# Kernel tuning notes

Hardware: AMD Instinct MI355X
Metric: run time of the kernel (lower is better)

The kernel has to match this reference:

```python
import jax, jax.numpy as jnp
import numpy as np

B, T, DIN, DC, CS = 8, 4096, 1024, 256, 8192
EPS = 1e-12

def _l2norm(x):
    # F.normalize: x / max(||x||_2, eps) along last axis
    n = jnp.sqrt(jnp.sum(x * x, axis=-1, keepdims=True))
    return x / jnp.maximum(n, EPS)

def _wn(v, g):
    # torch weight_norm(dim=0): w = g * v / ||v|| per output row
    n = jnp.sqrt(jnp.sum(v * v, axis=1, keepdims=True))
    return g * v / jnp.maximum(n, EPS)

def setup_inputs() -> dict:
    key = jax.random.key(0)
    k = jax.random.split(key, 4)
    return {
        "z": jax.random.normal(k[0], (B, DIN, T), jnp.float32),
        "in_v": jax.random.normal(k[1], (DC, DIN), jnp.float32) * 0.02,
        "in_g": jnp.ones((DC, 1), jnp.float32),
        "in_b": jnp.zeros((DC,), jnp.float32),
        "out_v": jax.random.normal(k[2], (DIN, DC), jnp.float32) * 0.02,
        "out_g": jnp.ones((DIN, 1), jnp.float32),
        "out_b": jnp.zeros((DIN,), jnp.float32),
        "codebook": jax.random.normal(k[3], (CS, DC), jnp.float32),
    }

def reference(z, in_v, in_g, in_b, out_v, out_g, out_b, codebook):
    b, _, t = z.shape
    w_in = _wn(in_v, in_g)                      # (DC, DIN)
    z_e = jnp.einsum('bdt,cd->bct', z, w_in) + in_b[None, :, None]  # (B, DC, T)

    # decode_latents (eval mode: dropout p=0)
    enc = _l2norm(z_e.transpose(0, 2, 1).reshape(b * t, -1))   # (BT, DC)
    cb = _l2norm(codebook)                                     # (CS, DC)
    dist = (jnp.sum(enc * enc, axis=1, keepdims=True)
            - 2.0 * enc @ cb.T
            + jnp.sum(cb * cb, axis=1)[None, :])               # (BT, CS)
    indices = jnp.argmax(-dist, axis=1).reshape(b, t)          # (B, T)
    z_q = codebook[indices].transpose(0, 2, 1)                 # (B, DC, T)

    commitment_loss = jnp.mean((z_e - jax.lax.stop_gradient(z_q)) ** 2, axis=(1, 2))
    codebook_loss = jnp.mean((z_q - jax.lax.stop_gradient(z_e)) ** 2, axis=(1, 2))

    z_q_st = z_e + jax.lax.stop_gradient(z_q - z_e)            # straight-through
    w_out = _wn(out_v, out_g)                                  # (DIN, DC)
    z_q_out = jnp.einsum('bct,dc->bdt', z_q_st, w_out) + out_b[None, :, None]
    return (z_q_out, commitment_loss, codebook_loss, indices)
```

## Files before the change

### kernel.cpp

```cpp
#include <hip/hip_runtime.h>
#include <stdint.h>

#define BB 8
#define TT 4096
#define DIN 1024
#define DC 256
#define CS 8192
#define EPSF 1e-12f

typedef unsigned short ushort_t;
typedef __attribute__((ext_vector_type(8))) short short8;
typedef __attribute__((ext_vector_type(4))) float f32x4;

constexpr size_t OFF_WIN   = 0;
constexpr size_t OFF_WOUTT = OFF_WIN   + 1048576;
constexpr size_t OFF_CBN   = OFF_WOUTT + 1048576;
constexpr size_t OFF_NRM2  = OFF_CBN   + 8388608;
constexpr size_t OFF_ZE    = OFF_NRM2  + 32768;
constexpr size_t OFF_INV   = OFF_ZE    + 33554432;
constexpr size_t OFF_ENC2  = OFF_INV   + 131072;
constexpr size_t OFF_KEYS  = OFF_ENC2  + 131072;
constexpr size_t OFF_LOSS  = OFF_KEYS  + 262144;
constexpr size_t OFF_WSPL  = OFF_LOSS  + 256;
constexpr size_t OFF_W2T   = OFF_WSPL  + 1048576;
constexpr size_t REQ_WS_ZE = OFF_W2T + 134217728ull;

__device__ __forceinline__ float block_reduce_sum_256(float v, float* sbuf) {
  #pragma unroll
  for (int o = 32; o > 0; o >>= 1) v += __shfl_down(v, o, 64);
  int lane = threadIdx.x & 63, w = threadIdx.x >> 6;
  if (lane == 0) sbuf[w] = v;
  __syncthreads();
  float r = sbuf[0] + sbuf[1] + sbuf[2] + sbuf[3];
  __syncthreads();
  return r;
}

__device__ __forceinline__ ushort_t bf16_rne(float x) {
  unsigned u = __float_as_uint(x);
  unsigned r = (u + 0x7FFFu + ((u >> 16) & 1u)) >> 16;
  return (ushort_t)r;
}
__device__ __forceinline__ float bf16f(ushort_t h) {
  return __uint_as_float(((unsigned)h) << 16);
}

__device__ __forceinline__ void async_copy16(const ushort_t* g, ushort_t* lds) {
  __builtin_amdgcn_global_load_lds(
      (const __attribute__((address_space(1))) void*)g,
      (__attribute__((address_space(3))) void*)lds, 16, 0, 0);
}

__device__ __forceinline__ void stage_tile(const ushort_t* __restrict__ s0, int ld,
                                           ushort_t* __restrict__ dstbuf, int rr, int cc) {
  #pragma unroll
  for (int r16 = 0; r16 < 8; r16++) {
    int r = r16*16 + rr;
    int g = cc ^ ((r + (r >> 2)) & 3);
    async_copy16(s0 + (size_t)r*ld + (g << 3), dstbuf + r16*512);
  }
}

__device__ __forceinline__ void stage_comp(const ushort_t* __restrict__ src,
                                           ushort_t* __restrict__ comp, int tid) {
  const int lane = tid & 63;
  const int wb = tid - lane;
  #pragma unroll
  for (int l = 0; l < 2; l++) {
    int chunk = l*512 + wb + lane;
    int r = chunk >> 2, c = chunk & 3;
    int g = c ^ ((r + (r >> 2)) & 3);
    async_copy16(src + (size_t)r*DC + (g << 3),
                 comp + (size_t)(l*512 + wb)*8);
  }
}

#define LD8(base, off) (*(const short8*)((const char*)(base) + (off)))

template<int MH, int CLO>
__device__ __forceinline__ void qmfma(f32x4 (&acc)[8][4],
    const short8 (&fah)[4], const short8 (&fal)[4],
    const short8 (&fbh)[4], const short8 (&fbl)[4]) {
  #pragma unroll
  for (int r = 0; r < 4; r++) {
    #pragma unroll
    for (int c2 = 0; c2 < 2; c2++) {
      f32x4 t = acc[MH*4 + r][CLO + c2];
      t = __builtin_amdgcn_mfma_f32_16x16x32_bf16(fah[r], fbh[CLO + c2], t, 0, 0, 0);
      t = __builtin_amdgcn_mfma_f32_16x16x32_bf16(fal[r], fbh[CLO + c2], t, 0, 0, 0);
      t = __builtin_amdgcn_mfma_f32_16x16x32_bf16(fah[r], fbl[CLO + c2], t, 0, 0, 0);
      acc[MH*4 + r][CLO + c2] = t;
    }
  }
}

__global__ void k_prep_win(const float* __restrict__ v, const float* __restrict__ g,
                           float* __restrict__ w, ushort_t* __restrict__ wh,
                           ushort_t* __restrict__ wl) {
  __shared__ float sb[4];
  int r = blockIdx.x, t = threadIdx.x;
  float xv[4]; float s = 0.f;
  #pragma unroll
  for (int i = 0; i < 4; i++) { xv[i] = v[r*DIN + t + i*256]; s += xv[i]*xv[i]; }
  s = block_reduce_sum_256(s, sb);
  float sc = g[r] / fmaxf(sqrtf(s), EPSF);
  #pragma unroll
  for (int i = 0; i < 4; i++) {
    float val = xv[i] * sc;
    int idx = r*DIN + t + i*256;
    w[idx] = val;
    ushort_t h = bf16_rne(val);
    wh[idx] = h;
    wl[idx] = bf16_rne(val - bf16f(h));
  }
}

__global__ void k_prep_wout(const float* __restrict__ v, const float* __restrict__ g,
                            float* __restrict__ wT) {
  __shared__ float sb[4];
  int r = blockIdx.x, t = threadIdx.x;
  float x = v[r*DC + t];
  float s = block_reduce_sum_256(x*x, sb);
  float sc = g[r] / fmaxf(sqrtf(s), EPSF);
  wT[t*DIN + r] = x * sc;
}

__global__ void k_prep_cb(const float* __restrict__ cb, ushort_t* __restrict__ cbh,
                          ushort_t* __restrict__ cbl, float* __restrict__ nrm2) {
  __shared__ float sb[4];
  int j = blockIdx.x, t = threadIdx.x;
  float x = cb[j*DC + t];
  float s = block_reduce_sum_256(x*x, sb);
  float nm = fmaxf(sqrtf(s), EPSF);
  float cn = x / nm;
  ushort_t h = bf16_rne(cn);
  cbh[j*DC + t] = h;
  cbl[j*DC + t] = bf16_rne(cn - bf16f(h));
  float q = block_reduce_sum_256(cn*cn, sb);
  if (t == 0) nrm2[j] = q;
}

template<bool BIAS>
__global__ __launch_bounds__(256) void k_gemm(
    const float* __restrict__ A, const float* __restrict__ Bmat,
    const float* __restrict__ bias, float* __restrict__ C,
    int K, int lda, int ldb, int ldc, size_t strideB, size_t strideC)
{
  __shared__ float As[16][132];
  __shared__ float Bs[16][132];
  const int bn = blockIdx.x * 128;
  const int bm = blockIdx.y * 128;
  const float* Bb = Bmat + (size_t)blockIdx.z * strideB;
  float* Cb = C + (size_t)blockIdx.z * strideC;
  const int tid = threadIdx.x;
  const int tx = tid & 15, ty = tid >> 4;
  const int am = tid & 127, akq = (tid >> 7) * 8;
  const int bk = tid >> 5, bj = (tid & 31) * 4;

  float acc[8][8];
  #pragma unroll
  for (int i = 0; i < 8; i++)
    #pragma unroll
    for (int j = 0; j < 8; j++) acc[i][j] = 0.f;

  for (int k0 = 0; k0 < K; k0 += 16) {
    float4 a0 = *(const float4*)&A[(size_t)(bm+am)*lda + k0 + akq];
    float4 a1 = *(const float4*)&A[(size_t)(bm+am)*lda + k0 + akq + 4];
    float4 b0 = *(const float4*)&Bb[(size_t)(k0+bk)*ldb + bn + bj];
    float4 b1 = *(const float4*)&Bb[(size_t)(k0+bk+8)*ldb + bn + bj];
    As[akq+0][am] = a0.x; As[akq+1][am] = a0.y; As[akq+2][am] = a0.z; As[akq+3][am] = a0.w;
    As[akq+4][am] = a1.x; As[akq+5][am] = a1.y; As[akq+6][am] = a1.z; As[akq+7][am] = a1.w;
    *(float4*)&Bs[bk][bj] = b0;
    *(float4*)&Bs[bk+8][bj] = b1;
    __syncthreads();
    #pragma unroll
    for (int k = 0; k < 16; k++) {
      float av[8], bv[8];
      float4 x0 = *(const float4*)&As[k][tx*4];
      float4 x1 = *(const float4*)&As[k][tx*4+64];
      float4 y0 = *(const float4*)&Bs[k][ty*4];
      float4 y1 = *(const float4*)&Bs[k][ty*4+64];
      av[0]=x0.x; av[1]=x0.y; av[2]=x0.z; av[3]=x0.w;
      av[4]=x1.x; av[5]=x1.y; av[6]=x1.z; av[7]=x1.w;
      bv[0]=y0.x; bv[1]=y0.y; bv[2]=y0.z; bv[3]=y0.w;
      bv[4]=y1.x; bv[5]=y1.y; bv[6]=y1.z; bv[7]=y1.w;
      #pragma unroll
      for (int i = 0; i < 8; i++)
        #pragma unroll
        for (int j = 0; j < 8; j++)
          acc[i][j] += av[i] * bv[j];
    }
    __syncthreads();
  }

  #pragma unroll
  for (int i = 0; i < 8; i++) {
    int mm = bm + ((i < 4) ? tx*4 + i : 64 + tx*4 + (i-4));
    float bia = BIAS ? bias[mm] : 0.f;
    float4 v0 = make_float4(acc[i][0]+bia, acc[i][1]+bia, acc[i][2]+bia, acc[i][3]+bia);
    float4 v1 = make_float4(acc[i][4]+bia, acc[i][5]+bia, acc[i][6]+bia, acc[i][7]+bia);
    *(float4*)&Cb[(size_t)mm*ldc + bn + ty*4]      = v0;
    *(float4*)&Cb[(size_t)mm*ldc + bn + 64 + ty*4] = v1;
  }
}

__global__ void k_split_z(const float* __restrict__ z, ushort_t* __restrict__ zhi,
                          ushort_t* __restrict__ zlo) {
  __shared__ float tile[64][65];
  int b = blockIdx.z, t0 = blockIdx.x * 64, d0 = blockIdx.y * 64;
  int tx = threadIdx.x & 63, ty = threadIdx.x >> 6;
  const float* zb = z + (size_t)b*DIN*TT;
  #pragma unroll
  for (int i = 0; i < 16; i++) {
    int d = i*4 + ty;
    tile[d][tx] = zb[(size_t)(d0+d)*TT + t0 + tx];
  }
  __syncthreads();
  #pragma unroll
  for (int i = 0; i < 16; i++) {
    int t = i*4 + ty;
    float val = tile[tx][t];
    ushort_t h = bf16_rne(val);
    size_t o = ((size_t)(b*TT + t0 + t))*DIN + d0 + tx;
    zhi[o] = h;
    zlo[o] = bf16_rne(val - bf16f(h));
  }
}

__global__ __launch_bounds__(256) void k_ze_mfma(
    const ushort_t* __restrict__ zth, const ushort_t* __restrict__ ztl,
    const ushort_t* __restrict__ wh, const ushort_t* __restrict__ wl,
    const float* __restrict__ in_b, float* __restrict__ ze)
{
  __shared__ ushort_t As_hi[2][4096];
  __shared__ ushort_t As_lo[2][4096];
  __shared__ ushort_t Bs_hi[2][4096];
  __shared__ ushort_t Bs_lo[2][4096];

  const int b  = blockIdx.z;
  const int t0 = blockIdx.x * 128;
  const int c0 = blockIdx.y * 128;
  const int tid = threadIdx.x;
  const int lane = tid & 63;
  const int wave = tid >> 6;
  const int wr = wave >> 1, wc = wave & 1;
  const int m = lane & 15, quad = lane >> 4;

  const ushort_t* src; ushort_t* dst;
  {
    size_t aoff = ((size_t)(b*TT + t0)) * DIN;
    size_t boff = (size_t)c0 * DIN;
    if      (wave == 0) { src = zth + aoff; dst = &As_hi[0][0]; }
    else if (wave == 1) { src = ztl + aoff; dst = &As_lo[0][0]; }
    else if (wave == 2) { src = wh + boff;  dst = &Bs_hi[0][0]; }
    else                { src = wl + boff;  dst = &Bs_lo[0][0]; }
  }
  const int rr = lane >> 2, cc = lane & 3;

  int offA[4], offB[4];
  #pragma unroll
  for (int ri = 0; ri < 4; ri++) {
    int r = wr*64 + ri*16 + m;
    int p = quad ^ ((r + (r >> 2)) & 3);
    offA[ri] = r*64 + p*16;
  }
  #pragma unroll
  for (int ci = 0; ci < 4; ci++) {
    int r = wc*64 + ci*16 + m;
    int p = quad ^ ((r + (r >> 2)) & 3);
    offB[ci] = r*64 + p*16;
  }

  f32x4 acc[4][4];
  #pragma unroll
  for (int i = 0; i < 4; i++)
    #pragma unroll
    for (int j = 0; j < 4; j++) acc[i][j] = (f32x4)0.f;

  stage_tile(src, DIN, dst, rr, cc);

  for (int it = 0; it < 32; ++it) {
    __syncthreads();
    if (it < 31) stage_tile(src + (it+1)*32, DIN, dst + ((it+1)&1)*4096, rr, cc);
    const int bo = (it & 1) << 13;

    short8 bh[4], bl[4];
    #pragma unroll
    for (int ci = 0; ci < 4; ci++) {
      bh[ci] = *(const short8*)((const char*)Bs_hi + bo + offB[ci]);
      bl[ci] = *(const short8*)((const char*)Bs_lo + bo + offB[ci]);
    }
    #pragma unroll
    for (int ri = 0; ri < 4; ri++) {
      short8 ah = *(const short8*)((const char*)As_hi + bo + offA[ri]);
      short8 al = *(const short8*)((const char*)As_lo + bo + offA[ri]);
      #pragma unroll
      for (int ci = 0; ci < 4; ci++) {
        acc[ri][ci] = __builtin_amdgcn_mfma_f32_16x16x32_bf16(ah, bh[ci], acc[ri][ci], 0, 0, 0);
        acc[ri][ci] = __builtin_amdgcn_mfma_f32_16x16x32_bf16(al, bh[ci], acc[ri][ci], 0, 0, 0);
        acc[ri][ci] = __builtin_amdgcn_mfma_f32_16x16x32_bf16(ah, bl[ci], acc[ri][ci], 0, 0, 0);
      }
    }
  }

  #pragma unroll
  for (int ri = 0; ri < 4; ri++) {
    int t_loc = wr*64 + ri*16 + quad*4;
    #pragma unroll
    for (int ci = 0; ci < 4; ci++) {
      int c_loc = wc*64 + ci*16 + m;
      float bia = in_b[c0 + c_loc];
      float4 v = make_float4(acc[ri][ci][0]+bia, acc[ri][ci][1]+bia,
                             acc[ri][ci][2]+bia, acc[ri][ci][3]+bia);
      *(float4*)&ze[((size_t)b*DC + c0 + c_loc)*TT + t0 + t_loc] = v;
    }
  }
}

__global__ void k_colnorm(const float* __restrict__ ze, float* __restrict__ inv,
                          float* __restrict__ enc2) {
  int r = blockIdx.x * 256 + threadIdx.x;
  int b = r >> 12, t = r & 4095;
  const float* p = ze + (size_t)b*DC*TT + t;
  float s = 0.f;
  for (int c = 0; c < DC; c++) { float x = p[(size_t)c*TT]; s += x*x; }
  float iv = 1.f / fmaxf(sqrtf(s), EPSF);
  inv[r] = iv;
  enc2[r] = (s * iv) * iv;
}

__global__ void k_split_enc(const float* __restrict__ ze, const float* __restrict__ inv,
                            ushort_t* __restrict__ ehi, ushort_t* __restrict__ elo) {
  __shared__ float tile[64][65];
  int b = blockIdx.z, t0 = blockIdx.x * 64, c0 = blockIdx.y * 64;
  int tx = threadIdx.x & 63, ty = threadIdx.x >> 6;
  const float* zb = ze + (size_t)b*DC*TT;
  #pragma unroll
  for (int i = 0; i < 16; i++) {
    int c = i*4 + ty;
    tile[c][tx] = zb[(size_t)(c0+c)*TT + t0 + tx];
  }
  __syncthreads();
  #pragma unroll
  for (int i = 0; i < 16; i++) {
    int t = i*4 + ty;
    float iv = inv[b*TT + t0 + t];
    float val = tile[tx][t] * iv;
    ushort_t h = bf16_rne(val);
    size_t o = ((size_t)(b*TT + t0 + t))*DC + c0 + tx;
    ehi[o] = h;
    elo[o] = bf16_rne(val - bf16f(h));
  }
}

__global__ __launch_bounds__(512, 2) void k_dist_mfma(
    const ushort_t* __restrict__ ehi, const ushort_t* __restrict__ elo,
    const ushort_t* __restrict__ cbh, const ushort_t* __restrict__ cbl,
    const float* __restrict__ nrm2, const float* __restrict__ enc2,
    unsigned long long* __restrict__ keys)
{
  __shared__ ushort_t sAh[2][8192];
  __shared__ ushort_t sAl[2][8192];
  __shared__ ushort_t sBh[2][8192];
  __shared__ ushort_t sBl[2][8192];
  __shared__ float sE2[256], sN2[256];
  __shared__ unsigned long long rkey[256];

  const int j0 = blockIdx.x * 256;
  const size_t r0 = (size_t)blockIdx.y * 256;
  const int tid = threadIdx.x;
  const int lane = tid & 63;
  const int wave = tid >> 6;
  const int wr = wave >> 2, wc = wave & 3;
  const int ml = lane & 15, quad = lane >> 4;

  if (tid < 256) {
    sE2[tid] = enc2[r0 + tid];
    sN2[tid] = nrm2[j0 + tid];
    rkey[tid] = 0xFFFFFFFFFFFFFFFFull;
  }

  const ushort_t* gAh = ehi + r0 * DC;
  const ushort_t* gAl = elo + r0 * DC;
  const ushort_t* gBh = cbh + (size_t)j0 * DC;
  const ushort_t* gBl = cbl + (size_t)j0 * DC;

  int offA[8], offB[4];
  #pragma unroll
  for (int i = 0; i < 8; i++) {
    int r = wr*128 + i*16 + ml;
    int p = quad ^ ((r + (r >> 2)) & 3);
    offA[i] = r*64 + p*16;
  }
  #pragma unroll
  for (int i = 0; i < 4; i++) {
    int r = wc*64 + i*16 + ml;
    int p = quad ^ ((r + (r >> 2)) & 3);
    offB[i] = r*64 + p*16;
  }

  f32x4 acc[8][4];
  #pragma unroll
  for (int i = 0; i < 8; i++)
    #pragma unroll
    for (int j = 0; j < 4; j++) acc[i][j] = (f32x4)0.f;

  stage_comp(gBh,      &sBh[0][0], tid);
  stage_comp(gBl,      &sBl[0][0], tid);
  stage_comp(gAh,      &sAh[0][0], tid);
  stage_comp(gAl,      &sAl[0][0], tid);
  stage_comp(gBh + 32, &sBh[1][0], tid);
  stage_comp(gBl + 32, &sBl[1][0], tid);
  asm volatile("s_waitcnt vmcnt(4)" ::: "memory");
  asm volatile("s_waitcnt lgkmcnt(0)" ::: "memory");
  __builtin_amdgcn_s_barrier();
  __builtin_amdgcn_sched_barrier(0);

  short8 fa_h[4], fa_l[4], fb_h[4], fb_l[4];

  #pragma unroll 2
  for (int k = 0; k < 8; k++) {
    const int cb = k & 1, nb = cb ^ 1;
    const char* pAh = (const char*)&sAh[cb][0];
    const char* pAl = (const char*)&sAl[cb][0];
    const char* pBh = (const char*)&sBh[cb][0];
    const char* pBl = (const char*)&sBl[cb][0];
    __builtin_amdgcn_sched_barrier(0);

    #pragma unroll
    for (int i = 0; i < 4; i++) { fa_h[i] = LD8(pAh, offA[i]); fa_l[i] = LD8(pAl, offA[i]); }
    #pragma unroll
    for (int i = 0; i < 2; i++) { fb_h[i] = LD8(pBh, offB[i]); fb_l[i] = LD8(pBl, offB[i]); }
    if (k < 7) stage_comp(gAh + (size_t)(k+1)*32, &sAh[nb][0], tid);
    __builtin_amdgcn_s_barrier();
    __builtin_amdgcn_s_setprio(1);
    qmfma<0, 0>(acc, fa_h, fa_l, fb_h, fb_l);
    __builtin_amdgcn_s_setprio(0);
    __builtin_amdgcn_s_barrier();

    #pragma unroll
    for (int i = 2; i < 4; i++) { fb_h[i] = LD8(pBh, offB[i]); fb_l[i] = LD8(pBl, offB[i]); }
    if (k < 7) stage_comp(gAl + (size_t)(k+1)*32, &sAl[nb][0], tid);
    __builtin_amdgcn_s_barrier();
    __builtin_amdgcn_s_setprio(1);
    qmfma<0, 2>(acc, fa_h, fa_l, fb_h, fb_l);
    __builtin_amdgcn_s_setprio(0);
    __builtin_amdgcn_s_barrier();

    #pragma unroll
    for (int i = 0; i < 4; i++) { fa_h[i] = LD8(pAh, offA[4+i]); fa_l[i] = LD8(pAl, offA[4+i]); }
    if (k < 6) stage_comp(gBh + (size_t)(k+2)*32, &sBh[cb][0], tid);
    __builtin_amdgcn_s_barrier();
    __builtin_amdgcn_s_setprio(1);
    qmfma<1, 2>(acc, fa_h, fa_l, fb_h, fb_l);
    __builtin_amdgcn_s_setprio(0);
    __builtin_amdgcn_s_barrier();

    if (k < 6) stage_comp(gBl + (size_t)(k+2)*32, &sBl[cb][0], tid);
    __builtin_amdgcn_s_barrier();
    __builtin_amdgcn_s_setprio(1);
    qmfma<1, 0>(acc, fa_h, fa_l, fb_h, fb_l);
    __builtin_amdgcn_s_setprio(0);
    if (k < 6) { asm volatile("s_waitcnt vmcnt(4)" ::: "memory"); }
    else       { asm volatile("s_waitcnt vmcnt(0)" ::: "memory"); }
    __builtin_amdgcn_s_barrier();
  }

  #pragma unroll
  for (int ri = 0; ri < 8; ri++) {
    #pragma unroll
    for (int reg = 0; reg < 4; reg++) {
      int t_loc = wr*128 + ri*16 + quad*4 + reg;
      float e2 = sE2[t_loc];
      unsigned long long best = 0xFFFFFFFFFFFFFFFFull;
      #pragma unroll
      for (int ci = 0; ci < 4; ci++) {
        int j_loc = wc*64 + ci*16 + ml;
        float d = e2 - 2.0f * acc[ri][ci][reg];
        d = d + sN2[j_loc];
        unsigned long long key =
            ((unsigned long long)__float_as_uint(d) << 32) | (unsigned)(j0 + j_loc);
        best = key < best ? key : best;
      }
      #pragma unroll
      for (int off = 1; off < 16; off <<= 1) {
        unsigned long long o = __shfl_xor(best, off);
        best = o < best ? o : best;
      }
      if (ml == 0) atomicMin(&rkey[t_loc], best);
    }
  }
  __syncthreads();
  if (tid < 256) atomicMin(&keys[r0 + tid], rkey[tid]);
}

__global__ void k_lossidx(const float* __restrict__ ze, const float* __restrict__ cb,
                          const unsigned long long* __restrict__ keys,
                          float* __restrict__ loss_sums, float* __restrict__ out_idx)
{
  __shared__ float sb[4];
  __shared__ int sj[64];
  int b = blockIdx.y, t0 = blockIdx.x * 64;
  int tid = threadIdx.x;
  if (tid < 64) {
    unsigned long long k = keys[(size_t)b*TT + t0 + tid];
    int j = (int)(unsigned)(k & 0xFFFFFFFFull);
    sj[tid] = j;
    out_idx[(size_t)b*TT + t0 + tid] = (float)j;
  }
  __syncthreads();
  int tt = tid & 63, tc = tid >> 6;
  const float* zb = ze + (size_t)b*DC*TT + t0;
  int j = sj[tt];
  float s = 0.f;
  for (int ci = 0; ci < 64; ci++) {
    int c = tc + ci*4;
    float zev = zb[(size_t)c*TT + tt];
    float zqv = cb[(size_t)j*DC + c];
    float d = zev - zqv;
    s += d*d;
  }
  s = block_reduce_sum_256(s, sb);
  if (tid == 0) atomicAdd(&loss_sums[b], s);
}

__global__ void k_losswrite(const float* __restrict__ loss_sums, float* __restrict__ out_loss) {
  int i = threadIdx.x;
  if (i < 8) {
    float v = loss_sums[i] * (1.f/1048576.f);
    out_loss[i] = v;
    out_loss[8 + i] = v;
  }
}

__global__ void k_outgather(const float* __restrict__ W2T,
                            const unsigned long long* __restrict__ keys,
                            const float* __restrict__ out_b, float* __restrict__ out)
{
  __shared__ float tile[64][65];
  __shared__ int sj[64];
  int b = blockIdx.y, t0 = blockIdx.x * 64;
  int tid = threadIdx.x;
  if (tid < 64) sj[tid] = (int)(unsigned)(keys[(size_t)b*TT + t0 + tid] & 0xFFFFFFFFull);
  __syncthreads();
  float* ob = out + (size_t)b*DIN*TT;
  int dd = tid & 63, tq = tid >> 6;
  for (int d0 = 0; d0 < DIN; d0 += 64) {
    #pragma unroll
    for (int i = 0; i < 16; i++) {
      int t = tq*16 + i;
      tile[t][dd] = W2T[(size_t)sj[t]*DIN + d0 + dd];
    }
    __syncthreads();
    #pragma unroll
    for (int i = 0; i < 16; i++) {
      int d = tq*16 + i;
      ob[(size_t)(d0+d)*TT + t0 + dd] = tile[dd][d] + out_b[d0+d];
    }
    __syncthreads();
  }
}

extern "C" void kernel_launch(void* const* d_in, const int* in_sizes, int n_in,
                              void* d_out, int out_size, void* d_ws, size_t ws_size,
                              hipStream_t stream) {
  const float* z        = (const float*)d_in[0];
  const float* in_v     = (const float*)d_in[1];
  const float* in_g     = (const float*)d_in[2];
  const float* in_b     = (const float*)d_in[3];
  const float* out_v    = (const float*)d_in[4];
  const float* out_g    = (const float*)d_in[5];
  const float* out_b    = (const float*)d_in[6];
  const float* codebook = (const float*)d_in[7];

  char* w = (char*)d_ws;
  float* w_in   = (float*)(w + OFF_WIN);
  float* w_outT = (float*)(w + OFF_WOUTT);
  ushort_t* cb_hi = (ushort_t*)(w + OFF_CBN);
  ushort_t* cb_lo = cb_hi + (size_t)CS*DC;
  float* nrm2   = (float*)(w + OFF_NRM2);
  float* z_e    = (float*)(w + OFF_ZE);
  float* inv    = (float*)(w + OFF_INV);
  float* enc2   = (float*)(w + OFF_ENC2);
  unsigned long long* keys = (unsigned long long*)(w + OFF_KEYS);
  float* loss_sums = (float*)(w + OFF_LOSS);
  ushort_t* w_hi = (ushort_t*)(w + OFF_WSPL);
  ushort_t* w_lo = w_hi + (size_t)DC*DIN;
  ushort_t* zt_hi = (ushort_t*)(w + OFF_W2T);
  ushort_t* zt_lo = zt_hi + (size_t)BB*TT*DIN;
  ushort_t* enc_hi = (ushort_t*)(w + OFF_W2T);
  ushort_t* enc_lo = enc_hi + (size_t)BB*TT*DC;
  float* W2T    = (float*)(w + OFF_W2T);

  float* out      = (float*)d_out;
  float* out_loss = out + (size_t)BB*DIN*TT;
  float* out_idx  = out_loss + 16;

  hipMemsetAsync(keys, 0xFF, 32768ull*8, stream);
  hipMemsetAsync(loss_sums, 0, 32, stream);

  k_prep_win <<<256, 256, 0, stream>>>(in_v, in_g, w_in, w_hi, w_lo);
  k_prep_wout<<<1024, 256, 0, stream>>>(out_v, out_g, w_outT);
  k_prep_cb  <<<8192, 256, 0, stream>>>(codebook, cb_hi, cb_lo, nrm2);

  if (ws_size >= REQ_WS_ZE) {
    k_split_z<<<dim3(64, 16, 8), 256, 0, stream>>>(z, zt_hi, zt_lo);
    k_ze_mfma<<<dim3(32, 2, 8), 256, 0, stream>>>(zt_hi, zt_lo, w_hi, w_lo, in_b, z_e);
  } else {
    k_gemm<true><<<dim3(32, 2, 8), 256, 0, stream>>>(
        w_in, z, in_b, z_e, 1024, 1024, 4096, 4096,
        (size_t)DIN*TT, (size_t)DC*TT);
  }

  k_colnorm<<<128, 256, 0, stream>>>(z_e, inv, enc2);
  k_split_enc<<<dim3(64, 4, 8), 256, 0, stream>>>(z_e, inv, enc_hi, enc_lo);

  k_dist_mfma<<<dim3(32, 128), 512, 0, stream>>>(
      enc_hi, enc_lo, cb_hi, cb_lo, nrm2, enc2, keys);

  k_gemm<false><<<dim3(8, 64, 1), 256, 0, stream>>>(
      codebook, w_outT, nullptr, W2T, 256, 256, 1024, 1024,
      (size_t)0, (size_t)0);

  k_lossidx<<<dim3(64, 8), 256, 0, stream>>>(z_e, codebook, keys, loss_sums, out_idx);
  k_losswrite<<<1, 64, 0, stream>>>(loss_sums, out_loss);
  k_outgather<<<dim3(64, 8), 256, 0, stream>>>(W2T, keys, out_b, out);
}
```

Baseline: 911.3 us.

## Use split-bf16 MFMA for codebook×Wout GEMM, retune dist kernel swizzle and argmin reduction

Replaces the fp32 SIMT GEMM that builds the codebook-times-Wout table with a 3-pass split-bf16 MFMA kernel, adding small kernels that split the raw codebook and normalized Wout into hi/lo halves. The LDS swizzle is changed to also mix in r>>3, aimed at reducing bank conflicts. The distance kernel merges two staging/barrier phases into one, which removes a barrier pair per k-step. Its argmin reduction now writes per-lane candidates to LDS instead of running a full shuffle tree plus LDS atomics. The new code adds extra launches and workspace traffic, and the split-bf16 products could differ slightly from fp32.

```diff
diff --git a/kernel.cpp b/kernel.cpp
--- a/kernel.cpp
+++ b/kernel.cpp
@@ -45,6 +45,10 @@
   return __uint_as_float(((unsigned)h) << 16);
 }
 
+__device__ __forceinline__ int swz4(int r) {
+  return (r + (r >> 2) + (r >> 3)) & 3;
+}
+
 __device__ __forceinline__ void async_copy16(const ushort_t* g, ushort_t* lds) {
   __builtin_amdgcn_global_load_lds(
       (const __attribute__((address_space(1))) void*)g,
@@ -56,7 +60,7 @@
   #pragma unroll
   for (int r16 = 0; r16 < 8; r16++) {
     int r = r16*16 + rr;
-    int g = cc ^ ((r + (r >> 2)) & 3);
+    int g = cc ^ swz4(r);
     async_copy16(s0 + (size_t)r*ld + (g << 3), dstbuf + r16*512);
   }
 }
@@ -69,7 +73,7 @@
   for (int l = 0; l < 2; l++) {
     int chunk = l*512 + wb + lane;
     int r = chunk >> 2, c = chunk & 3;
-    int g = c ^ ((r + (r >> 2)) & 3);
+    int g = c ^ swz4(r);
     async_copy16(src + (size_t)r*DC + (g << 3),
                  comp + (size_t)(l*512 + wb)*8);
   }
@@ -138,6 +142,28 @@
   cbl[j*DC + t] = bf16_rne(cn - bf16f(h));
   float q = block_reduce_sum_256(cn*cn, sb);
   if (t == 0) nrm2[j] = q;
+}
+
+__global__ void k_split_cbraw(const float* __restrict__ cb, ushort_t* __restrict__ ch,
+                              ushort_t* __restrict__ cl) {
+  int j = blockIdx.x, t = threadIdx.x;
+  float x = cb[j*DC + t];
+  ushort_t h = bf16_rne(x);
+  ch[j*DC + t] = h;
+  cl[j*DC + t] = bf16_rne(x - bf16f(h));
+}
+
+__global__ void k_split_wout(const float* __restrict__ v, const float* __restrict__ g,
+                             ushort_t* __restrict__ wh, ushort_t* __restrict__ wl) {
+  __shared__ float sb[4];
+  int r = blockIdx.x, t = threadIdx.x;
+  float x = v[r*DC + t];
+  float s = block_reduce_sum_256(x*x, sb);
+  float sc = g[r] / fmaxf(sqrtf(s), EPSF);
+  float val = x * sc;
+  ushort_t h = bf16_rne(val);
+  wh[r*DC + t] = h;
+  wl[r*DC + t] = bf16_rne(val - bf16f(h));
 }
 
 template<bool BIAS>
@@ -261,13 +287,13 @@
   #pragma unroll
   for (int ri = 0; ri < 4; ri++) {
     int r = wr*64 + ri*16 + m;
-    int p = quad ^ ((r + (r >> 2)) & 3);
+    int p = quad ^ swz4(r);
     offA[ri] = r*64 + p*16;
   }
   #pragma unroll
   for (int ci = 0; ci < 4; ci++) {
     int r = wc*64 + ci*16 + m;
-    int p = quad ^ ((r + (r >> 2)) & 3);
+    int p = quad ^ swz4(r);
     offB[ci] = r*64 + p*16;
   }
 
@@ -313,6 +339,95 @@
       float4 v = make_float4(acc[ri][ci][0]+bia, acc[ri][ci][1]+bia,
                              acc[ri][ci][2]+bia, acc[ri][ci][3]+bia);
       *(float4*)&ze[((size_t)b*DC + c0 + c_loc)*TT + t0 + t_loc] = v;
+    }
+  }
+}
+
+__global__ __launch_bounds__(256) void k_w2t_mfma(
+    const ushort_t* __restrict__ ah_g, const ushort_t* __restrict__ al_g,
+    const ushort_t* __restrict__ bh_g, const ushort_t* __restrict__ bl_g,
+    float* __restrict__ C)
+{
+  __shared__ ushort_t As_hi[2][4096];
+  __shared__ ushort_t As_lo[2][4096];
+  __shared__ ushort_t Bs_hi[2][4096];
+  __shared__ ushort_t Bs_lo[2][4096];
+
+  const int m0 = blockIdx.x * 128;
+  const int n0 = blockIdx.y * 128;
+  const int tid = threadIdx.x;
+  const int lane = tid & 63;
+  const int wave = tid >> 6;
+  const int wr = wave >> 1, wc = wave & 1;
+  const int m = lane & 15, quad = lane >> 4;
+
+  const ushort_t* src; ushort_t* dst;
+  {
+    size_t aoff = (size_t)m0 * DC;
+    size_t boff = (size_t)n0 * DC;
+    if      (wave == 0) { src = ah_g + aoff; dst = &As_hi[0][0]; }
+    else if (wave == 1) { src = al_g + aoff; dst = &As_lo[0][0]; }
+    else if (wave == 2) { src = bh_g + boff; dst = &Bs_hi[0][0]; }
+    else                { src = bl_g + boff; dst = &Bs_lo[0][0]; }
+  }
+  const int rr = lane >> 2, cc = lane & 3;
+
+  int offA[4], offB[4];
+  #pragma unroll
+  for (int ri = 0; ri < 4; ri++) {
+    int r = wr*64 + ri*16 + m;
+    int p = quad ^ swz4(r);
+    offA[ri] = r*64 + p*16;
+  }
+  #pragma unroll
+  for (int ci = 0; ci < 4; ci++) {
+    int r = wc*64 + ci*16 + m;
+    int p = quad ^ swz4(r);
+    offB[ci] = r*64 + p*16;
+  }
+
+  f32x4 acc[4][4];
+  #pragma unroll
+  for (int i = 0; i < 4; i++)
+    #pragma unroll
+    for (int j = 0; j < 4; j++) acc[i][j] = (f32x4)0.f;
+
+  stage_tile(src, DC, dst, rr, cc);
+
+  for (int it = 0; it < 8; ++it) {
+    __syncthreads();
+    if (it < 7) stage_tile(src + (it+1)*32, DC, dst + ((it+1)&1)*4096, rr, cc);
+    const int bo = (it & 1) << 13;
+
+    short8 bh[4], bl[4];
+    #pragma unroll
+    for (int ci = 0; ci < 4; ci++) {
+      bh[ci] = *(const short8*)((const char*)Bs_hi + bo + offB[ci]);
+      bl[ci] = *(const short8*)((const char*)Bs_lo + bo + offB[ci]);
+    }
+    #pragma unroll
+    for (int ri = 0; ri < 4; ri++) {
+      short8 ah = *(const short8*)((const char*)As_hi + bo + offA[ri]);
+      short8 al = *(const short8*)((const char*)As_lo + bo + offA[ri]);
+      #pragma unroll
+      for (int ci = 0; ci < 4; ci++) {
+        acc[ri][ci] = __builtin_amdgcn_mfma_f32_16x16x32_bf16(ah, bh[ci], acc[ri][ci], 0, 0, 0);
+        acc[ri][ci] = __builtin_amdgcn_mfma_f32_16x16x32_bf16(al, bh[ci], acc[ri][ci], 0, 0, 0);
+        acc[ri][ci] = __builtin_amdgcn_mfma_f32_16x16x32_bf16(ah, bl[ci], acc[ri][ci], 0, 0, 0);
+      }
+    }
+  }
+
+  #pragma unroll
+  for (int ri = 0; ri < 4; ri++) {
+    int m_loc = wr*64 + ri*16 + quad*4;
+    #pragma unroll
+    for (int ci = 0; ci < 4; ci++) {
+      int n_loc = wc*64 + ci*16 + m;
+      #pragma unroll
+      for (int reg = 0; reg < 4; reg++) {
+        C[(size_t)(m0 + m_loc + reg)*DIN + n0 + n_loc] = acc[ri][ci][reg];
+      }
     }
   }
 }
@@ -364,7 +479,6 @@
   __shared__ ushort_t sBh[2][8192];
   __shared__ ushort_t sBl[2][8192];
   __shared__ float sE2[256], sN2[256];
-  __shared__ unsigned long long rkey[256];
 
   const int j0 = blockIdx.x * 256;
   const size_t r0 = (size_t)blockIdx.y * 256;
@@ -377,7 +491,6 @@
   if (tid < 256) {
     sE2[tid] = enc2[r0 + tid];
     sN2[tid] = nrm2[j0 + tid];
-    rkey[tid] = 0xFFFFFFFFFFFFFFFFull;
   }
 
   const ushort_t* gAh = ehi + r0 * DC;
@@ -389,13 +502,13 @@
   #pragma unroll
   for (int i = 0; i < 8; i++) {
     int r = wr*128 + i*16 + ml;
-    int p = quad ^ ((r + (r >> 2)) & 3);
+    int p = quad ^ swz4(r);
     offA[i] = r*64 + p*16;
   }
   #pragma unroll
   for (int i = 0; i < 4; i++) {
     int r = wc*64 + i*16 + ml;
-    int p = quad ^ ((r + (r >> 2)) & 3);
+    int p = quad ^ swz4(r);
     offB[i] = r*64 + p*16;
   }
 
@@ -449,16 +562,13 @@
 
     #pragma unroll
     for (int i = 0; i < 4; i++) { fa_h[i] = LD8(pAh, offA[4+i]); fa_l[i] = LD8(pAl, offA[4+i]); }
-    if (k < 6) stage_comp(gBh + (size_t)(k+2)*32, &sBh[cb][0], tid);
+    if (k < 6) {
+      stage_comp(gBh + (size_t)(k+2)*32, &sBh[cb][0], tid);
+      stage_comp(gBl + (size_t)(k+2)*32, &sBl[cb][0], tid);
+    }
     __builtin_amdgcn_s_barrier();
     __builtin_amdgcn_s_setprio(1);
     qmfma<1, 2>(acc, fa_h, fa_l, fb_h, fb_l);
-    __builtin_amdgcn_s_setprio(0);
-    __builtin_amdgcn_s_barrier();
-
-    if (k < 6) stage_comp(gBl + (size_t)(k+2)*32, &sBl[cb][0], tid);
-    __builtin_amdgcn_s_barrier();
-    __builtin_amdgcn_s_setprio(1);
     qmfma<1, 0>(acc, fa_h, fa_l, fb_h, fb_l);
     __builtin_amdgcn_s_setprio(0);
     if (k < 6) { asm volatile("s_waitcnt vmcnt(4)" ::: "memory"); }
@@ -466,6 +576,7 @@
     __builtin_amdgcn_s_barrier();
   }
 
+  unsigned long long* cand = (unsigned long long*)&sAh[0][0];
   #pragma unroll
   for (int ri = 0; ri < 8; ri++) {
     #pragma unroll
@@ -482,16 +593,21 @@
             ((unsigned long long)__float_as_uint(d) << 32) | (unsigned)(j0 + j_loc);
         best = key < best ? key : best;
       }
-      #pragma unroll
-      for (int off = 1; off < 16; off <<= 1) {
-        unsigned long long o = __shfl_xor(best, off);
-        best = o < best ? o : best;
-      }
-      if (ml == 0) atomicMin(&rkey[t_loc], best);
+      unsigned long long o1 = __shfl_xor(best, 1); best = o1 < best ? o1 : best;
+      unsigned long long o2 = __shfl_xor(best, 2); best = o2 < best ? o2 : best;
+      if ((ml & 3) == 0) cand[t_loc*16 + wc*4 + (ml >> 2)] = best;
     }
   }
   __syncthreads();
-  if (tid < 256) atomicMin(&keys[r0 + tid], rkey[tid]);
+  if (tid < 256) {
+    unsigned long long b = 0xFFFFFFFFFFFFFFFFull;
+    #pragma unroll
+    for (int s = 0; s < 16; s++) {
+      unsigned long long v = cand[tid*16 + s];
+      b = v < b ? v : b;
+    }
+    atomicMin(&keys[r0 + tid], b);
+  }
 }
 
 __global__ void k_lossidx(const float* __restrict__ ze, const float* __restrict__ cb,
@@ -591,6 +707,10 @@
   ushort_t* enc_hi = (ushort_t*)(w + OFF_W2T);
   ushort_t* enc_lo = enc_hi + (size_t)BB*TT*DC;
   float* W2T    = (float*)(w + OFF_W2T);
+  ushort_t* cbr_hi  = (ushort_t*)(w + OFF_W2T + 33554432);
+  ushort_t* cbr_lo  = cbr_hi + (size_t)CS*DC;
+  ushort_t* wout_hi = (ushort_t*)(w + OFF_W2T + 33554432 + 8388608);
+  ushort_t* wout_lo = wout_hi + (size_t)DIN*DC;
 
   float* out      = (float*)d_out;
   float* out_loss = out + (size_t)BB*DIN*TT;
@@ -599,14 +719,16 @@
   hipMemsetAsync(keys, 0xFF, 32768ull*8, stream);
   hipMemsetAsync(loss_sums, 0, 32, stream);
 
+  const bool mfma_path = (ws_size >= REQ_WS_ZE);
+
   k_prep_win <<<256, 256, 0, stream>>>(in_v, in_g, w_in, w_hi, w_lo);
-  k_prep_wout<<<1024, 256, 0, stream>>>(out_v, out_g, w_outT);
   k_prep_cb  <<<8192, 256, 0, stream>>>(codebook, cb_hi, cb_lo, nrm2);
 
-  if (ws_size >= REQ_WS_ZE) {
+  if (mfma_path) {
     k_split_z<<<dim3(64, 16, 8), 256, 0, stream>>>(z, zt_hi, zt_lo);
     k_ze_mfma<<<dim3(32, 2, 8), 256, 0, stream>>>(zt_hi, zt_lo, w_hi, w_lo, in_b, z_e);
   } else {
+    k_prep_wout<<<1024, 256, 0, stream>>>(out_v, out_g, w_outT);
     k_gemm<true><<<dim3(32, 2, 8), 256, 0, stream>>>(
         w_in, z, in_b, z_e, 1024, 1024, 4096, 4096,
         (size_t)DIN*TT, (size_t)DC*TT);
@@ -618,11 +740,18 @@
   k_dist_mfma<<<dim3(32, 128), 512, 0, stream>>>(
       enc_hi, enc_lo, cb_hi, cb_lo, nrm2, enc2, keys);
 
-  k_gemm<false><<<dim3(8, 64, 1), 256, 0, stream>>>(
-      codebook, w_outT, nullptr, W2T, 256, 256, 1024, 1024,
-      (size_t)0, (size_t)0);
-
   k_lossidx<<<dim3(64, 8), 256, 0, stream>>>(z_e, codebook, keys, loss_sums, out_idx);
   k_losswrite<<<1, 64, 0, stream>>>(loss_sums, out_loss);
+
+  if (mfma_path) {
+    k_split_cbraw<<<8192, 256, 0, stream>>>(codebook, cbr_hi, cbr_lo);
+    k_split_wout <<<1024, 256, 0, stream>>>(out_v, out_g, wout_hi, wout_lo);
+    k_w2t_mfma<<<dim3(64, 8), 256, 0, stream>>>(cbr_hi, cbr_lo, wout_hi, wout_lo, W2T);
+  } else {
+    k_gemm<false><<<dim3(8, 64, 1), 256, 0, stream>>>(
+        codebook, w_outT, nullptr, W2T, 256, 256, 1024, 1024,
+        (size_t)0, (size_t)0);
+  }
+
   k_outgather<<<dim3(64, 8), 256, 0, stream>>>(W2T, keys, out_b, out);
 }
```

Measured after the change: 912.2 us. No clear change (+0.1%).
